# Kernel tuning notes

Hardware: AMD Instinct MI355X
Metric: run time of the kernel (lower is better)

Reference implementation:

```python
import jax, jax.numpy as jnp
import numpy as np

MAX_REL = 30  # hardcoded in SpatialVelocityCrossAttention (rel_pos_enc max_rel_pos=30)
N_HEADS = 8


def conv1d_same(x, w, b):
    # x: [B, L, Cin], w: [O, I, K] (torch layout), b: [O]; 'same' padding for odd K
    k = w.shape[-1]
    y = jax.lax.conv_general_dilated(
        x, jnp.transpose(w, (2, 1, 0)), (1,), [(k // 2, k // 2)],
        dimension_numbers=('NHC', 'HIO', 'NHC'))
    return y + b


def rel_pos_enc(xm, emb, dw_w, dw_b):
    # Faithful closed form of RelativePositionalEncoding.forward.
    # fused[b,i,j] = xm[b,j] + emb[clip(j-i,-R,R)+R]; depthwise 3-tap conv along j per row i;
    # output[b,j] = mean_i( conv_out if i==j else fused ) =
    #   xm[b,j] + (sum_i pos[i,j] - (xm[b,j]+emb[R]) + diag_conv[b,j]) / S
    B, S, D = xm.shape
    r = jnp.arange(S)
    idx = jnp.clip(r[None, :] - r[:, None], -MAX_REL, MAX_REL) + MAX_REL  # [i, j]
    counts = (idx[:, :, None] == jnp.arange(2 * MAX_REL + 1)[None, None, :]).sum(0)  # [j, 2R+1]
    pos_sum = counts.astype(xm.dtype) @ emb  # [S, D] = sum_i emb[clip(j-i)+R]
    fC = xm + emb[MAX_REL]                      # fused[b,j,j]
    # padded-conv neighbors of the diagonal (zero input outside sequence):
    fL = jnp.pad(xm[:, :-1] + emb[MAX_REL - 1], ((0, 0), (1, 0), (0, 0)))  # fused[b,j,j-1]
    fR = jnp.pad(xm[:, 1:] + emb[MAX_REL + 1], ((0, 0), (0, 1), (0, 0)))   # fused[b,j,j+1]
    diag_conv = fL * dw_w[:, 0] + fC * dw_w[:, 1] + fR * dw_w[:, 2] + dw_b
    return xm + (pos_sum[None] - fC + diag_conv) / S


def setup_inputs() -> dict:
    key = jax.random.key(0)
    ks = jax.random.split(key, 16)
    B, L, MN = 32, 1024, 512           # L == 2*MN (required by Gamma.repeat(1,2,1))
    sd, vd, dm = 256, 64, 256          # spatial_dim == d_model (residual add), velocity_dim
    d3 = 3 * vd

    def w(k, shape, s=0.05):
        return jax.random.normal(k, shape, jnp.float32) * s

    return {
        'x_spatial': jax.random.normal(ks[0], (B, L, sd), jnp.float32),
        'x_velocity': jax.random.normal(ks[1], (B, MN, vd), jnp.float32),
        'Wg': w(ks[2], (dm, vd)),                 # conv_gamma (1x1, no bias)
        'ms_w3': w(ks[3], (vd, vd, 3)), 'ms_b3': jnp.zeros((vd,), jnp.float32),
        'ms_w5': w(ks[4], (vd, vd, 5)), 'ms_b5': jnp.zeros((vd,), jnp.float32),
        'ms_w7': w(ks[5], (vd, vd, 7)), 'ms_b7': jnp.zeros((vd,), jnp.float32),
        'rel_emb': w(ks[6], (2 * MAX_REL + 1, d3)),
        'dw_w': w(ks[7], (d3, 3), 0.1), 'dw_b': jnp.zeros((d3,), jnp.float32),
        'Wq': w(ks[8], (dm, sd)),
        'Wk': w(ks[9], (dm, d3)),
        'Wv': w(ks[10], (dm, d3)),
        'fc_w': w(ks[11], (dm, dm)), 'fc_b': jnp.zeros((dm,), jnp.float32),
        'ln_w': jnp.ones((dm,), jnp.float32), 'ln_b': jnp.zeros((dm,), jnp.float32),
    }


def reference(x_spatial, x_velocity, Wg, ms_w3, ms_b3, ms_w5, ms_b5, ms_w7, ms_b7,
              rel_emb, dw_w, dw_b, Wq, Wk, Wv, fc_w, fc_b, ln_w, ln_b):
    B, L, sd = x_spatial.shape
    _, MN, vd = x_velocity.shape
    dm = Wq.shape[0]
    H, dk = N_HEADS, Wq.shape[0] // N_HEADS

    # sigmoid-gated 1x1 conv on velocity
    Gamma = jax.nn.sigmoid(jnp.einsum('bsc,dc->bsd', x_velocity, Wg))  # [B, MN, dm]

    # multi-scale convs, concat on channel -> [B, MN, 3*vd]
    xm = jnp.concatenate([
        conv1d_same(x_velocity, ms_w3, ms_b3),
        conv1d_same(x_velocity, ms_w5, ms_b5),
        conv1d_same(x_velocity, ms_w7, ms_b7)], axis=-1)

    x_v_pe = rel_pos_enc(xm, rel_emb, dw_w, dw_b)  # [B, MN, 3*vd]

    # 1x1-conv Q/K/V projections, split heads channel-major (matches torch view)
    Q = jnp.einsum('blc,dc->bld', x_spatial, Wq).reshape(B, L, H, dk).transpose(0, 2, 1, 3)
    K = jnp.einsum('bsc,dc->bsd', x_v_pe, Wk).reshape(B, MN, H, dk).transpose(0, 2, 1, 3)
    V = jnp.einsum('bsc,dc->bsd', x_v_pe, Wv).reshape(B, MN, H, dk).transpose(0, 2, 1, 3)

    attn = jax.nn.softmax(jnp.einsum('bhld,bhsd->bhls', Q, K) / np.sqrt(dk).astype(np.float32), axis=-1)
    out = jnp.einsum('bhls,bhsd->bhld', attn, V)           # [B, H, L, dk]
    out = out.transpose(0, 2, 1, 3).reshape(B, L, dm)       # concat heads
    out = out @ fc_w.T + fc_b

    out = jnp.tile(Gamma, (1, 2, 1)) * out                  # Gamma.repeat(1,2,1) gating
    x = x_spatial + out
    mu = x.mean(-1, keepdims=True)
    var = x.var(-1, keepdims=True)
    return (x - mu) / jnp.sqrt(var + 1e-5) * ln_w + ln_b
```

## Files before the change

### kernel.cpp

```cpp
#include <hip/hip_runtime.h>

#define B   32
#define L   1024
#define MN  512
#define SD  256
#define VD  64
#define DM  256
#define D3  192
#define NH  8
#define DK  32
#define RMAX 30
#define NREL 61
#define SPAD 518

typedef __attribute__((ext_vector_type(8))) __bf16 bf16x8;
typedef __attribute__((ext_vector_type(4))) float  f32x4;

static __device__ __forceinline__ ushort f2bf(float f) {
  unsigned u = __float_as_uint(f);
  unsigned r = (u + 0x7FFFu + ((u >> 16) & 1u)) >> 16;
  return (ushort)r;
}
static __device__ __forceinline__ bf16x8 ldbf8(const ushort* p) {
  return __builtin_bit_cast(bf16x8, *(const uint4*)p);
}
static __device__ __forceinline__ float fexp2(float x) {
  return __builtin_amdgcn_exp2f(x);
}

__global__ __launch_bounds__(256) void prep_kernel(
    const float* __restrict__ Wg, ushort* __restrict__ Wgb,
    const float* __restrict__ Wq, ushort* __restrict__ Wqb,
    const float* __restrict__ Wk, ushort* __restrict__ Wkb,
    const float* __restrict__ Wv, ushort* __restrict__ Wvb,
    const float* __restrict__ fcw, ushort* __restrict__ fcwb,
    const float* __restrict__ xv, ushort* __restrict__ xp,
    const float* __restrict__ w3, const float* __restrict__ w5,
    const float* __restrict__ w7, ushort* __restrict__ wb,
    const float* __restrict__ emb, float* __restrict__ psum) {
  int blk = blockIdx.x;
  if (blk < 240) {
    const float* s; ushort* d; int base;
    if (blk < 16)       { s = Wg;  d = Wgb;  base = blk; }
    else if (blk < 80)  { s = Wq;  d = Wqb;  base = blk - 16; }
    else if (blk < 128) { s = Wk;  d = Wkb;  base = blk - 80; }
    else if (blk < 176) { s = Wv;  d = Wvb;  base = blk - 128; }
    else                { s = fcw; d = fcwb; base = blk - 176; }
    int i = (base * 256 + threadIdx.x) * 4;
    float4 v = *(const float4*)(s + i);
    *(ushort4*)(d + i) = make_ushort4(f2bf(v.x), f2bf(v.y), f2bf(v.z), f2bf(v.w));
  } else if (blk < 240 + 4144) {
    int i = (blk - 240) * 256 + threadIdx.x;
    if (i < B * SPAD * VD) {
      int c = i & 63;
      int bp = i >> 6;
      int b_ = bp / SPAD, p = bp - b_ * SPAD;
      int s = p - 3;
      float v = (s >= 0 && s < MN) ? xv[((size_t)b_ * MN + s) * VD + c] : 0.f;
      ushort hi = f2bf(v);
      float vh = __uint_as_float((uint)hi << 16);
      ushort lo = f2bf(v - vh);
      xp[i] = hi;
      xp[(size_t)B * SPAD * VD + i] = lo;
    }
  } else if (blk < 240 + 4144 + 192) {
    const int o = blk - (240 + 4144);
    const int scale = o >> 6, oo = o & 63;
    for (int j = threadIdx.x; j < 448; j += 256) {
      const int k7 = j >> 6, i = j & 63;
      float v = 0.f;
      if (scale == 0) {
        int k = k7 - 2; if (k >= 0 && k < 3) v = w3[((size_t)oo * VD + i) * 3 + k];
      } else if (scale == 1) {
        int k = k7 - 1; if (k >= 0 && k < 5) v = w5[((size_t)oo * VD + i) * 5 + k];
      } else {
        v = w7[((size_t)oo * VD + i) * 7 + k7];
      }
      wb[(size_t)o * 448 + j] = f2bf(v);
    }
  } else {
    const int j = blk - (240 + 4144 + 192);
    const int d = threadIdx.x;
    if (d < D3) {
      float acc = 0.f;
      for (int r = 0; r < NREL; ++r) {
        int v = r - RMAX;
        int cnt;
        if (r == 0)             cnt = max(0, MN - (j + RMAX));
        else if (r == NREL - 1) cnt = max(0, j - RMAX + 1);
        else                    cnt = (j - v >= 0 && j - v < MN) ? 1 : 0;
        acc += (float)cnt * emb[(size_t)r * D3 + d];
      }
      psum[(size_t)j * D3 + d] = acc;
    }
  }
}

template<int CIN, int OMODE, int ACT, int AF32>
static __device__ __forceinline__ void proj_body(
    int blk, const void* __restrict__ Xv, const ushort* __restrict__ Wb,
    void* __restrict__ Yv, int tid) {
  const int wave = tid >> 6, lane = tid & 63;
  const int q15 = lane & 15, quad = lane >> 4;
  const int row0 = blk * 64 + wave * 16;
  constexpr int KS = CIN / 32;

  f32x4 acc[16];
#pragma unroll
  for (int t = 0; t < 16; ++t) acc[t] = (f32x4){0.f, 0.f, 0.f, 0.f};

  const ushort* abase = (const ushort*)Xv + (size_t)(row0 + q15) * CIN + quad * 8;
  const float*  fbase = (const float*)Xv + (size_t)(row0 + q15) * CIN + quad * 8;
  const ushort* bbase = Wb + (size_t)q15 * CIN + quad * 8;
#pragma unroll 2
  for (int ks = 0; ks < KS; ++ks) {
    bf16x8 af;
    if constexpr (AF32) {
      float4 u0 = *(const float4*)(fbase + ks * 32);
      float4 u1 = *(const float4*)(fbase + ks * 32 + 4);
      uint4 p;
      p.x = (uint)f2bf(u0.x) | ((uint)f2bf(u0.y) << 16);
      p.y = (uint)f2bf(u0.z) | ((uint)f2bf(u0.w) << 16);
      p.z = (uint)f2bf(u1.x) | ((uint)f2bf(u1.y) << 16);
      p.w = (uint)f2bf(u1.z) | ((uint)f2bf(u1.w) << 16);
      af = __builtin_bit_cast(bf16x8, p);
    } else {
      af = ldbf8(abase + ks * 32);
    }
#pragma unroll
    for (int t = 0; t < 16; ++t) {
      bf16x8 bf = ldbf8(bbase + (size_t)t * 16 * CIN + ks * 32);
      acc[t] = __builtin_amdgcn_mfma_f32_16x16x32_bf16(af, bf, acc[t], 0, 0, 0);
    }
  }
#pragma unroll
  for (int reg = 0; reg < 4; ++reg) {
    const int row = row0 + quad * 4 + reg;
#pragma unroll
    for (int t = 0; t < 16; ++t) {
      int col = t * 16 + q15;
      float v = acc[t][reg];
      if (ACT == 1) v = 1.f / (1.f + __expf(-v));
      if (OMODE == 0) {
        ((float*)Yv)[(size_t)row * DM + col] = v;
      } else {
        int b_ = row >> 10, q = row & 1023;
        int h = col >> 5, dk = col & 31;
        ((ushort*)Yv)[((size_t)((b_ * NH + h) * L + q)) * DK + dk] = f2bf(v);
      }
    }
  }
}

static __device__ __forceinline__ void conv_body(
    int blk, const ushort* __restrict__ Xp, const ushort* __restrict__ Wb,
    const float* __restrict__ b3, const float* __restrict__ b5,
    const float* __restrict__ b7, float* __restrict__ xm, int tid) {
  const int wave = tid >> 6, lane = tid & 63;
  const int q15 = lane & 15, quad = lane >> 4;
  const int row0 = blk * 32;
  const int b_ = row0 >> 9, s0 = row0 & 511;

  f32x4 acc0[3], acc1[3];
#pragma unroll
  for (int t = 0; t < 3; ++t) {
    acc0[t] = (f32x4){0.f, 0.f, 0.f, 0.f};
    acc1[t] = (f32x4){0.f, 0.f, 0.f, 0.f};
  }
  const ushort* h0 = Xp + ((size_t)b_ * SPAD + s0 + q15) * VD + quad * 8;
  const ushort* h1 = h0 + 16 * VD;
  const ushort* l0 = h0 + (size_t)B * SPAD * VD;
  const ushort* l1 = l0 + 16 * VD;
  const ushort* wbase = Wb + ((size_t)wave * 48 + q15) * 448 + quad * 8;

#pragma unroll 2
  for (int ks = 0; ks < 14; ++ks) {
    bf16x8 ah0 = ldbf8(h0 + ks * 32), al0 = ldbf8(l0 + ks * 32);
    bf16x8 ah1 = ldbf8(h1 + ks * 32), al1 = ldbf8(l1 + ks * 32);
#pragma unroll
    for (int t = 0; t < 3; ++t) {
      bf16x8 bf = ldbf8(wbase + (size_t)t * 16 * 448 + ks * 32);
      acc0[t] = __builtin_amdgcn_mfma_f32_16x16x32_bf16(ah0, bf, acc0[t], 0, 0, 0);
      acc0[t] = __builtin_amdgcn_mfma_f32_16x16x32_bf16(al0, bf, acc0[t], 0, 0, 0);
      acc1[t] = __builtin_amdgcn_mfma_f32_16x16x32_bf16(ah1, bf, acc1[t], 0, 0, 0);
      acc1[t] = __builtin_amdgcn_mfma_f32_16x16x32_bf16(al1, bf, acc1[t], 0, 0, 0);
    }
  }
#pragma unroll
  for (int t = 0; t < 3; ++t) {
    const int col = (wave * 3 + t) * 16 + q15;
    const float bias = col < 64 ? b3[col] : (col < 128 ? b5[col - 64] : b7[col - 128]);
#pragma unroll
    for (int reg = 0; reg < 4; ++reg) {
      const int row = row0 + quad * 4 + reg;
      xm[(size_t)row * D3 + col] = acc0[t][reg] + bias;
      xm[(size_t)(row + 16) * D3 + col] = acc1[t][reg] + bias;
    }
  }
}

__global__ __launch_bounds__(256, 2) void mega1_kernel(
    const ushort* __restrict__ Xp, const ushort* __restrict__ Wbig,
    const float* __restrict__ b3, const float* __restrict__ b5,
    const float* __restrict__ b7, float* __restrict__ xm,
    const float* __restrict__ xv, const ushort* __restrict__ Wgb,
    float* __restrict__ Gamma,
    const float* __restrict__ xs, const ushort* __restrict__ Wqb,
    ushort* __restrict__ Qb) {
  const int blk = blockIdx.x;
  const int tid = threadIdx.x;
  if (blk < 512) {
    conv_body(blk, Xp, Wbig, b3, b5, b7, xm, tid);
  } else if (blk < 768) {
    proj_body<VD, 0, 1, 1>(blk - 512, xv, Wgb, Gamma, tid);
  } else {
    proj_body<SD, 4, 0, 1>(blk - 768, xs, Wqb, Qb, tid);
  }
}

#define PPAD 200
__global__ __launch_bounds__(256, 2) void projkv_pe_kernel(
    const float* __restrict__ xm, const float* __restrict__ psum,
    const float* __restrict__ emb, const float* __restrict__ dww,
    const float* __restrict__ dwb, const ushort* __restrict__ Wkb,
    const ushort* __restrict__ Wvb, ushort* __restrict__ Kp,
    ushort* __restrict__ Vt) {
  const int isV = blockIdx.x >> 8;
  const int blk = blockIdx.x & 255;
  const int tid = threadIdx.x;
  const int row0 = blk * 64;

  __shared__ ushort pes[64][PPAD];

#pragma unroll 2
  for (int it = 0; it < 12; ++it) {
    int f = it * 256 + tid;
    int r = f / 48, c4 = (f % 48) * 4;
    int grow = row0 + r;
    int j = grow & 511;
    const float* arow = xm + (size_t)grow * D3 + c4;
    f32x4 xc = *(const f32x4*)(arow);
    f32x4 xl = (j > 0)      ? *(const f32x4*)(arow - D3) : (f32x4){0.f, 0.f, 0.f, 0.f};
    f32x4 xr = (j < MN - 1) ? *(const f32x4*)(arow + D3) : (f32x4){0.f, 0.f, 0.f, 0.f};
    f32x4 ps = *(const f32x4*)(psum + (size_t)j * D3 + c4);
    f32x4 eC = *(const f32x4*)(emb + (size_t)RMAX * D3 + c4);
    f32x4 eL = *(const f32x4*)(emb + (size_t)(RMAX - 1) * D3 + c4);
    f32x4 eR = *(const f32x4*)(emb + (size_t)(RMAX + 1) * D3 + c4);
    ushort4 o;
    ushort* op = (ushort*)&o;
#pragma unroll
    for (int k = 0; k < 4; ++k) {
      int d = c4 + k;
      float fC = xc[k] + eC[k];
      float fL = (j > 0)      ? xl[k] + eL[k] : 0.f;
      float fR = (j < MN - 1) ? xr[k] + eR[k] : 0.f;
      float dc = fL * dww[d * 3 + 0] + fC * dww[d * 3 + 1] + fR * dww[d * 3 + 2] + dwb[d];
      op[k] = f2bf(xc[k] + (ps[k] - fC + dc) * (1.f / MN));
    }
    *(ushort4*)(&pes[r][c4]) = o;
  }
  __syncthreads();

  const int wave = tid >> 6, lane = tid & 63;
  const int q15 = lane & 15, quad = lane >> 4;
  const int wrow0 = row0 + wave * 16;

  f32x4 acc[16];
#pragma unroll
  for (int t = 0; t < 16; ++t) acc[t] = (f32x4){0.f, 0.f, 0.f, 0.f};

  const ushort* abase = &pes[wave * 16 + q15][quad * 8];
  const ushort* bbase = (isV ? Wvb : Wkb) + (size_t)q15 * D3 + quad * 8;
#pragma unroll 2
  for (int ks = 0; ks < 6; ++ks) {
    bf16x8 af = ldbf8(abase + ks * 32);
#pragma unroll
    for (int t = 0; t < 16; ++t) {
      bf16x8 bf = ldbf8(bbase + (size_t)t * 16 * D3 + ks * 32);
      acc[t] = __builtin_amdgcn_mfma_f32_16x16x32_bf16(af, bf, acc[t], 0, 0, 0);
    }
  }
#pragma unroll
  for (int reg = 0; reg < 4; ++reg) {
    const int row = wrow0 + quad * 4 + reg;
    const int b_ = row >> 9, s = row & 511;
#pragma unroll
    for (int t = 0; t < 16; ++t) {
      int col = t * 16 + q15;
      float v = acc[t][reg];
      if (isV) {
        int h = t >> 1, dk = (t & 1) * 16 + q15;
        Vt[((size_t)((b_ * NH + h) * DK + dk)) * MN + s] = f2bf(v);
      } else {
        int h = col >> 5, dk = col & 31;
        Kp[((size_t)((b_ * NH + h) * MN + s)) * DK + dk] = f2bf(v);
      }
    }
  }
}

#define PSTRIDE 36
__global__ __launch_bounds__(256, 3) void attn_mfma_kernel(
    const ushort* __restrict__ Qb, const ushort* __restrict__ Kb,
    const ushort* __restrict__ Vt, ushort* __restrict__ Ao) {
  const int blk = blockIdx.x;
  const int bh = blk & 255;
  const int qc = blk >> 8;
  const int h  = bh & 7;
  const int b_ = bh >> 3;
  const int tid = threadIdx.x;
  const int wave = tid >> 6, lane = tid & 63;
  const int q15 = lane & 15, quad = lane >> 4;
  const int q0 = qc * 128 + wave * 32;

  __shared__ ushort Plds[4][2][16][PSTRIDE];
  ushort* prowA = &Plds[wave][0][q15][0];
  ushort* prowB = &Plds[wave][1][q15][0];

  const ushort* qrow = Qb + ((size_t)((b_ * NH + h) * L) + q0 + q15) * DK + quad * 8;
  const bf16x8 qfA = ldbf8(qrow);
  const bf16x8 qfB = ldbf8(qrow + (size_t)16 * DK);

  f32x4 o0A = {0.f, 0.f, 0.f, 0.f}, o1A = {0.f, 0.f, 0.f, 0.f};
  f32x4 o0B = {0.f, 0.f, 0.f, 0.f}, o1B = {0.f, 0.f, 0.f, 0.f};
  float mA = -1e30f, lA = 0.f, mB = -1e30f, lB = 0.f;
  const float sc2 = 0.17677669529663687f * 1.4426950408889634f;

  const ushort* kbase = Kb + (((size_t)(b_ * NH + h) * MN) + q15) * DK + quad * 8;
  const ushort* vbase = Vt + ((size_t)((b_ * NH + h) * DK) + q15) * MN;

#pragma unroll
  for (int c = 0; c < 4; ++c) {
    const int kb0 = c * 128;
    bf16x8 av[8];
#pragma unroll
    for (int g = 0; g < 4; ++g) {
      av[g * 2]     = ldbf8(vbase + (size_t)(kb0 + g * 32 + quad * 8));
      av[g * 2 + 1] = ldbf8(vbase + (size_t)16 * MN + (kb0 + g * 32 + quad * 8));
    }
    f32x4 sA[8], sB[8];
#pragma unroll
    for (int t = 0; t < 8; ++t) {
      bf16x8 af = ldbf8(kbase + (size_t)(kb0 + t * 16) * DK);
      f32x4 z = {0.f, 0.f, 0.f, 0.f};
      sA[t] = __builtin_amdgcn_mfma_f32_16x16x32_bf16(af, qfA, z, 0, 0, 0);
      sB[t] = __builtin_amdgcn_mfma_f32_16x16x32_bf16(af, qfB, z, 0, 0, 0);
    }
    float mlA = -1e30f, mlB = -1e30f;
#pragma unroll
    for (int t = 0; t < 8; ++t)
#pragma unroll
      for (int r = 0; r < 4; ++r) {
        sA[t][r] *= sc2; mlA = fmaxf(mlA, sA[t][r]);
        sB[t][r] *= sc2; mlB = fmaxf(mlB, sB[t][r]);
      }
    mlA = fmaxf(mlA, __shfl_xor(mlA, 16));
    mlB = fmaxf(mlB, __shfl_xor(mlB, 16));
    mlA = fmaxf(mlA, __shfl_xor(mlA, 32));
    mlB = fmaxf(mlB, __shfl_xor(mlB, 32));
    float mnA = fmaxf(mA, mlA), mnB = fmaxf(mB, mlB);
    float aA = fexp2(mA - mnA), aB = fexp2(mB - mnB);
    mA = mnA; mB = mnB;
    lA *= aA; lB *= aB;
#pragma unroll
    for (int r = 0; r < 4; ++r) {
      o0A[r] *= aA; o1A[r] *= aA;
      o0B[r] *= aB; o1B[r] *= aB;
    }
#pragma unroll
    for (int g = 0; g < 4; ++g) {
#pragma unroll
      for (int tp = 0; tp < 2; ++tp) {
        int t = 2 * g + tp;
        float a0 = fexp2(sA[t][0] - mA), a1 = fexp2(sA[t][1] - mA);
        float a2 = fexp2(sA[t][2] - mA), a3 = fexp2(sA[t][3] - mA);
        lA += (a0 + a1) + (a2 + a3);
        uint uA01 = __builtin_amdgcn_perm(__float_as_uint(a1), __float_as_uint(a0), 0x07060302u);
        uint uA23 = __builtin_amdgcn_perm(__float_as_uint(a3), __float_as_uint(a2), 0x07060302u);
        *(uint2*)(prowA + tp * 16 + quad * 4) = make_uint2(uA01, uA23);
        float b0 = fexp2(sB[t][0] - mB), b1 = fexp2(sB[t][1] - mB);
        float b2 = fexp2(sB[t][2] - mB), b3 = fexp2(sB[t][3] - mB);
        lB += (b0 + b1) + (b2 + b3);
        uint uB01 = __builtin_amdgcn_perm(__float_as_uint(b1), __float_as_uint(b0), 0x07060302u);
        uint uB23 = __builtin_amdgcn_perm(__float_as_uint(b3), __float_as_uint(b2), 0x07060302u);
        *(uint2*)(prowB + tp * 16 + quad * 4) = make_uint2(uB01, uB23);
      }
      bf16x8 bfA = ldbf8(prowA + quad * 8);
      bf16x8 bfB = ldbf8(prowB + quad * 8);
      o0A = __builtin_amdgcn_mfma_f32_16x16x32_bf16(av[g * 2],     bfA, o0A, 0, 0, 0);
      o1A = __builtin_amdgcn_mfma_f32_16x16x32_bf16(av[g * 2 + 1], bfA, o1A, 0, 0, 0);
      o0B = __builtin_amdgcn_mfma_f32_16x16x32_bf16(av[g * 2],     bfB, o0B, 0, 0, 0);
      o1B = __builtin_amdgcn_mfma_f32_16x16x32_bf16(av[g * 2 + 1], bfB, o1B, 0, 0, 0);
    }
  }
  lA += __shfl_xor(lA, 16); lA += __shfl_xor(lA, 32);
  lB += __shfl_xor(lB, 16); lB += __shfl_xor(lB, 32);
  float rA = 1.f / lA, rB = 1.f / lB;
  ushort* obA = Ao + ((size_t)((b_ * NH + h) * L) + q0 + q15) * DK + quad * 4;
  *(ushort4*)(obA)      = make_ushort4(f2bf(o0A[0] * rA), f2bf(o0A[1] * rA),
                                       f2bf(o0A[2] * rA), f2bf(o0A[3] * rA));
  *(ushort4*)(obA + 16) = make_ushort4(f2bf(o1A[0] * rA), f2bf(o1A[1] * rA),
                                       f2bf(o1A[2] * rA), f2bf(o1A[3] * rA));
  ushort* obB = obA + (size_t)16 * DK;
  *(ushort4*)(obB)      = make_ushort4(f2bf(o0B[0] * rB), f2bf(o0B[1] * rB),
                                       f2bf(o0B[2] * rB), f2bf(o0B[3] * rB));
  *(ushort4*)(obB + 16) = make_ushort4(f2bf(o1B[0] * rB), f2bf(o1B[1] * rB),
                                       f2bf(o1B[2] * rB), f2bf(o1B[3] * rB));
}

__global__ __launch_bounds__(256, 2) void final_mfma_kernel(
    const ushort* __restrict__ Ao, const ushort* __restrict__ fcwb,
    const float* __restrict__ fcb, const float* __restrict__ G,
    const float* __restrict__ Xs, const float* __restrict__ lnw,
    const float* __restrict__ lnb, float* __restrict__ out) {
  const int tid = threadIdx.x;
  const int wave = tid >> 6, lane = tid & 63;
  const int q15 = lane & 15, quad = lane >> 4;
  const int row0 = blockIdx.x * 64 + wave * 16;
  const int brow = row0 >> 10;
  const int srow = (row0 & 1023) + q15;

  f32x4 acc[16];
#pragma unroll
  for (int t = 0; t < 16; ++t) acc[t] = (f32x4){0.f, 0.f, 0.f, 0.f};

  const ushort* abase = Ao + ((size_t)(brow * NH) * L + srow) * DK + quad * 8;
  const ushort* bbase = fcwb + (size_t)q15 * DM + quad * 8;
#pragma unroll 2
  for (int ks = 0; ks < 8; ++ks) {
    bf16x8 af = ldbf8(abase + (size_t)ks * L * DK);
#pragma unroll
    for (int t = 0; t < 16; ++t) {
      bf16x8 bf = ldbf8(bbase + (size_t)t * 16 * DM + ks * 32);
      acc[t] = __builtin_amdgcn_mfma_f32_16x16x32_bf16(af, bf, acc[t], 0, 0, 0);
    }
  }
#pragma unroll
  for (int reg = 0; reg < 4; ++reg) {
    const int grow = row0 + quad * 4 + reg;
    const int b_ = grow >> 10;
    const int gl = (grow & 1023) & 511;
    const float* gbase = G + ((size_t)b_ * MN + gl) * DM + q15;
    const float* xbase = Xs + (size_t)grow * SD + q15;
    float vv[16];
    float s1 = 0.f, s2 = 0.f;
#pragma unroll
    for (int t = 0; t < 16; ++t) {
      int col = t * 16 + q15;
      float fcv = acc[t][reg] + fcb[col];
      float v = xbase[t * 16] + gbase[t * 16] * fcv;
      vv[t] = v; s1 += v; s2 += v * v;
    }
    s1 += __shfl_xor(s1, 1); s2 += __shfl_xor(s2, 1);
    s1 += __shfl_xor(s1, 2); s2 += __shfl_xor(s2, 2);
    s1 += __shfl_xor(s1, 4); s2 += __shfl_xor(s2, 4);
    s1 += __shfl_xor(s1, 8); s2 += __shfl_xor(s2, 8);
    float mu = s1 * (1.f / DM);
    float var = s2 * (1.f / DM) - mu * mu;
    float rs = rsqrtf(var + 1e-5f);
    float* obase = out + (size_t)grow * DM + q15;
#pragma unroll
    for (int t = 0; t < 16; ++t) {
      int col = t * 16 + q15;
      obase[t * 16] = (vv[t] - mu) * rs * lnw[col] + lnb[col];
    }
  }
}

extern "C" void kernel_launch(void* const* d_in, const int* in_sizes, int n_in,
                              void* d_out, int out_size, void* d_ws, size_t ws_size,
                              hipStream_t stream) {
  const float* x_spatial  = (const float*)d_in[0];
  const float* x_velocity = (const float*)d_in[1];
  const float* Wg   = (const float*)d_in[2];
  const float* w3   = (const float*)d_in[3];
  const float* b3   = (const float*)d_in[4];
  const float* w5   = (const float*)d_in[5];
  const float* b5   = (const float*)d_in[6];
  const float* w7   = (const float*)d_in[7];
  const float* b7   = (const float*)d_in[8];
  const float* remb = (const float*)d_in[9];
  const float* dww  = (const float*)d_in[10];
  const float* dwb  = (const float*)d_in[11];
  const float* Wq   = (const float*)d_in[12];
  const float* Wk   = (const float*)d_in[13];
  const float* Wv   = (const float*)d_in[14];
  const float* fcw  = (const float*)d_in[15];
  const float* fcb  = (const float*)d_in[16];
  const float* lnw  = (const float*)d_in[17];
  const float* lnb  = (const float*)d_in[18];
  float* out = (float*)d_out;

  char* w8 = (char*)d_ws;
  float*  Gamma = (float*)(w8);
  float*  xm    = (float*)(w8 + 16777216);
  float*  psum  = (float*)(w8 + 29360128);
  ushort* Qb    = (ushort*)(w8 + 36044800);
  ushort* Kp    = (ushort*)(w8 + 52822016);
  ushort* Vt    = (ushort*)(w8 + 61210624);
  ushort* Ao    = (ushort*)(w8 + 69599232);
  ushort* fcwb  = (ushort*)(w8 + 86376448);
  ushort* Wgb   = (ushort*)(w8 + 105381888);
  ushort* Wqb   = (ushort*)(w8 + 105414656);
  ushort* Wkb   = (ushort*)(w8 + 105545728);
  ushort* Wvb   = (ushort*)(w8 + 105644032);
  ushort* xvp   = (ushort*)(w8 + 69599232);
  ushort* wbigb = (ushort*)(w8 + 69599232 + 4243456);

  prep_kernel<<<240 + 4144 + 192 + 512, 256, 0, stream>>>(
      Wg, Wgb, Wq, Wqb, Wk, Wkb, Wv, Wvb, fcw, fcwb,
      x_velocity, xvp, w3, w5, w7, wbigb, remb, psum);

  mega1_kernel<<<1280, 256, 0, stream>>>(
      xvp, wbigb, b3, b5, b7, xm,
      x_velocity, Wgb, Gamma, x_spatial, Wqb, Qb);

  projkv_pe_kernel<<<512, 256, 0, stream>>>(
      xm, psum, remb, dww, dwb, Wkb, Wvb, Kp, Vt);

  attn_mfma_kernel<<<B * NH * (L / 128), 256, 0, stream>>>(Qb, Kp, Vt, Ao);
  final_mfma_kernel<<<B * L / 64, 256, 0, stream>>>(Ao, fcwb, fcb, Gamma,
                                                    x_spatial, lnw, lnb, out);
}
```

Baseline: 349.1 us.

## Split conv into its own kernel and store Gamma gate in bf16

Moves the multi-scale conv out of the merged kernel into a standalone kernel with 16-row tiles and a higher occupancy bound, leaving Gamma and Q projections in a separate launch. Gamma is now stored as bf16 instead of fp32, which halves its write and read traffic in the final LayerNorm kernel. This adds an extra kernel launch and loses some precision on the gating values, and the smaller conv tile reloads the weights more often.

```diff
diff --git a/kernel.cpp b/kernel.cpp
--- a/kernel.cpp
+++ b/kernel.cpp
@@ -20,6 +20,9 @@
   unsigned u = __float_as_uint(f);
   unsigned r = (u + 0x7FFFu + ((u >> 16) & 1u)) >> 16;
   return (ushort)r;
+}
+static __device__ __forceinline__ float bf2f(ushort u) {
+  return __uint_as_float((uint)u << 16);
 }
 static __device__ __forceinline__ bf16x8 ldbf8(const ushort* p) {
   return __builtin_bit_cast(bf16x8, *(const uint4*)p);
@@ -142,7 +145,7 @@
       float v = acc[t][reg];
       if (ACT == 1) v = 1.f / (1.f + __expf(-v));
       if (OMODE == 0) {
-        ((float*)Yv)[(size_t)row * DM + col] = v;
+        ((ushort*)Yv)[(size_t)row * DM + col] = f2bf(v);
       } else {
         int b_ = row >> 10, q = row & 1023;
         int h = col >> 5, dk = col & 31;
@@ -152,69 +155,58 @@
   }
 }
 
-static __device__ __forceinline__ void conv_body(
-    int blk, const ushort* __restrict__ Xp, const ushort* __restrict__ Wb,
-    const float* __restrict__ b3, const float* __restrict__ b5,
-    const float* __restrict__ b7, float* __restrict__ xm, int tid) {
-  const int wave = tid >> 6, lane = tid & 63;
-  const int q15 = lane & 15, quad = lane >> 4;
-  const int row0 = blk * 32;
-  const int b_ = row0 >> 9, s0 = row0 & 511;
-
-  f32x4 acc0[3], acc1[3];
-#pragma unroll
-  for (int t = 0; t < 3; ++t) {
-    acc0[t] = (f32x4){0.f, 0.f, 0.f, 0.f};
-    acc1[t] = (f32x4){0.f, 0.f, 0.f, 0.f};
-  }
-  const ushort* h0 = Xp + ((size_t)b_ * SPAD + s0 + q15) * VD + quad * 8;
-  const ushort* h1 = h0 + 16 * VD;
-  const ushort* l0 = h0 + (size_t)B * SPAD * VD;
-  const ushort* l1 = l0 + 16 * VD;
-  const ushort* wbase = Wb + ((size_t)wave * 48 + q15) * 448 + quad * 8;
-
-#pragma unroll 2
-  for (int ks = 0; ks < 14; ++ks) {
-    bf16x8 ah0 = ldbf8(h0 + ks * 32), al0 = ldbf8(l0 + ks * 32);
-    bf16x8 ah1 = ldbf8(h1 + ks * 32), al1 = ldbf8(l1 + ks * 32);
-#pragma unroll
-    for (int t = 0; t < 3; ++t) {
-      bf16x8 bf = ldbf8(wbase + (size_t)t * 16 * 448 + ks * 32);
-      acc0[t] = __builtin_amdgcn_mfma_f32_16x16x32_bf16(ah0, bf, acc0[t], 0, 0, 0);
-      acc0[t] = __builtin_amdgcn_mfma_f32_16x16x32_bf16(al0, bf, acc0[t], 0, 0, 0);
-      acc1[t] = __builtin_amdgcn_mfma_f32_16x16x32_bf16(ah1, bf, acc1[t], 0, 0, 0);
-      acc1[t] = __builtin_amdgcn_mfma_f32_16x16x32_bf16(al1, bf, acc1[t], 0, 0, 0);
-    }
-  }
-#pragma unroll
-  for (int t = 0; t < 3; ++t) {
-    const int col = (wave * 3 + t) * 16 + q15;
-    const float bias = col < 64 ? b3[col] : (col < 128 ? b5[col - 64] : b7[col - 128]);
-#pragma unroll
-    for (int reg = 0; reg < 4; ++reg) {
-      const int row = row0 + quad * 4 + reg;
-      xm[(size_t)row * D3 + col] = acc0[t][reg] + bias;
-      xm[(size_t)(row + 16) * D3 + col] = acc1[t][reg] + bias;
-    }
-  }
-}
-
-__global__ __launch_bounds__(256, 2) void mega1_kernel(
-    const ushort* __restrict__ Xp, const ushort* __restrict__ Wbig,
-    const float* __restrict__ b3, const float* __restrict__ b5,
-    const float* __restrict__ b7, float* __restrict__ xm,
+__global__ __launch_bounds__(256, 2) void proj_gq_kernel(
     const float* __restrict__ xv, const ushort* __restrict__ Wgb,
-    float* __restrict__ Gamma,
+    ushort* __restrict__ Gamma,
     const float* __restrict__ xs, const ushort* __restrict__ Wqb,
     ushort* __restrict__ Qb) {
   const int blk = blockIdx.x;
   const int tid = threadIdx.x;
-  if (blk < 512) {
-    conv_body(blk, Xp, Wbig, b3, b5, b7, xm, tid);
-  } else if (blk < 768) {
-    proj_body<VD, 0, 1, 1>(blk - 512, xv, Wgb, Gamma, tid);
+  if (blk < 256) {
+    proj_body<VD, 0, 1, 1>(blk, xv, Wgb, Gamma, tid);
   } else {
-    proj_body<SD, 4, 0, 1>(blk - 768, xs, Wqb, Qb, tid);
+    proj_body<SD, 4, 0, 1>(blk - 256, xs, Wqb, Qb, tid);
+  }
+}
+
+__global__ __launch_bounds__(256, 4) void conv_mfma_kernel(
+    const ushort* __restrict__ Xp, const ushort* __restrict__ Wb,
+    const float* __restrict__ b3, const float* __restrict__ b5,
+    const float* __restrict__ b7, float* __restrict__ xm) {
+  const int tid = threadIdx.x;
+  const int wave = tid >> 6, lane = tid & 63;
+  const int q15 = lane & 15, quad = lane >> 4;
+  const int row0 = blockIdx.x * 16;
+  const int b_ = row0 >> 9, s0 = row0 & 511;
+
+  f32x4 acc[3];
+#pragma unroll
+  for (int t = 0; t < 3; ++t) acc[t] = (f32x4){0.f, 0.f, 0.f, 0.f};
+
+  const ushort* hbase = Xp + ((size_t)b_ * SPAD + s0 + q15) * VD + quad * 8;
+  const ushort* lbase = hbase + (size_t)B * SPAD * VD;
+  const ushort* wbase = Wb + ((size_t)wave * 48 + q15) * 448 + quad * 8;
+
+#pragma unroll 2
+  for (int ks = 0; ks < 14; ++ks) {
+    bf16x8 ah = ldbf8(hbase + ks * 32);
+    bf16x8 al = ldbf8(lbase + ks * 32);
+#pragma unroll
+    for (int t = 0; t < 3; ++t) {
+      bf16x8 bf = ldbf8(wbase + (size_t)t * 16 * 448 + ks * 32);
+      acc[t] = __builtin_amdgcn_mfma_f32_16x16x32_bf16(ah, bf, acc[t], 0, 0, 0);
+      acc[t] = __builtin_amdgcn_mfma_f32_16x16x32_bf16(al, bf, acc[t], 0, 0, 0);
+    }
+  }
+#pragma unroll
+  for (int t = 0; t < 3; ++t) {
+    const int col = (wave * 3 + t) * 16 + q15;
+    const float bias = col < 64 ? b3[col] : (col < 128 ? b5[col - 64] : b7[col - 128]);
+#pragma unroll
+    for (int reg = 0; reg < 4; ++reg) {
+      const int row = row0 + quad * 4 + reg;
+      xm[(size_t)row * D3 + col] = acc[t][reg] + bias;
+    }
   }
 }
 
@@ -410,7 +402,7 @@
 
 __global__ __launch_bounds__(256, 2) void final_mfma_kernel(
     const ushort* __restrict__ Ao, const ushort* __restrict__ fcwb,
-    const float* __restrict__ fcb, const float* __restrict__ G,
+    const float* __restrict__ fcb, const ushort* __restrict__ G,
     const float* __restrict__ Xs, const float* __restrict__ lnw,
     const float* __restrict__ lnb, float* __restrict__ out) {
   const int tid = threadIdx.x;
@@ -440,7 +432,7 @@
     const int grow = row0 + quad * 4 + reg;
     const int b_ = grow >> 10;
     const int gl = (grow & 1023) & 511;
-    const float* gbase = G + ((size_t)b_ * MN + gl) * DM + q15;
+    const ushort* gbase = G + ((size_t)b_ * MN + gl) * DM + q15;
     const float* xbase = Xs + (size_t)grow * SD + q15;
     float vv[16];
     float s1 = 0.f, s2 = 0.f;
@@ -448,7 +440,7 @@
     for (int t = 0; t < 16; ++t) {
       int col = t * 16 + q15;
       float fcv = acc[t][reg] + fcb[col];
-      float v = xbase[t * 16] + gbase[t * 16] * fcv;
+      float v = xbase[t * 16] + bf2f(gbase[t * 16]) * fcv;
       vv[t] = v; s1 += v; s2 += v * v;
     }
     s1 += __shfl_xor(s1, 1); s2 += __shfl_xor(s2, 1);
@@ -492,7 +484,7 @@
   float* out = (float*)d_out;
 
   char* w8 = (char*)d_ws;
-  float*  Gamma = (float*)(w8);
+  ushort* Gamma = (ushort*)(w8);
   float*  xm    = (float*)(w8 + 16777216);
   float*  psum  = (float*)(w8 + 29360128);
   ushort* Qb    = (ushort*)(w8 + 36044800);
@@ -511,8 +503,9 @@
       Wg, Wgb, Wq, Wqb, Wk, Wkb, Wv, Wvb, fcw, fcwb,
       x_velocity, xvp, w3, w5, w7, wbigb, remb, psum);
 
-  mega1_kernel<<<1280, 256, 0, stream>>>(
-      xvp, wbigb, b3, b5, b7, xm,
+  conv_mfma_kernel<<<B * MN / 16, 256, 0, stream>>>(xvp, wbigb, b3, b5, b7, xm);
+
+  proj_gq_kernel<<<768, 256, 0, stream>>>(
       x_velocity, Wgb, Gamma, x_spatial, Wqb, Qb);
 
   projkv_pe_kernel<<<512, 256, 0, stream>>>(
```

After: 348.7 us. Within noise of the previous version (-0.1%).
